# Kernel tuning notes

Hardware: AMD Instinct MI355X
Metric: run time of the kernel (lower is better)

Reference implementation:

```python
import jax, jax.numpy as jnp
from jax import lax
import numpy as np

B, T, H = 128, 512, 512  # batch, seq_length, hidden_dim (== input_dim)


def _xavier(key, shape):
    fan_in, fan_out = shape[1], shape[0]
    limit = float(np.sqrt(6.0 / (fan_in + fan_out)))
    return jax.random.uniform(key, shape, jnp.float32, -limit, limit)


def setup_inputs() -> dict:
    key = jax.random.key(0)
    ks = jax.random.split(key, 10)
    s = 1.0 / np.sqrt(H)  # torch LSTM default init range
    return {
        "x": jax.random.normal(ks[0], (B, T, H), jnp.float32),
        "W_ih": jax.random.uniform(ks[1], (4 * H, H), jnp.float32, -s, s),
        "W_hh": jax.random.uniform(ks[2], (4 * H, H), jnp.float32, -s, s),
        "b_ih": jax.random.uniform(ks[3], (4 * H,), jnp.float32, -s, s),
        "b_hh": jax.random.uniform(ks[4], (4 * H,), jnp.float32, -s, s),
        "Ve": _xavier(ks[5], (1, H)),
        "U1": _xavier(ks[6], (H, 2 * H)),
        "U2": _xavier(ks[7], (H, H)),
        "W_out": _xavier(ks[8], (2, H)),
        "b_out": jnp.zeros((2,), jnp.float32),
    }


def _lstm(x, W_ih, W_hh, b_ih, b_hh):
    # x: [B, T, D] -> hidden states [B, T, H]; PyTorch gate order i,f,g,o
    b = b_ih + b_hh
    # precompute input projections for all timesteps: [T, B, 4H]
    xg = jnp.einsum('btd,gd->tbg', x, W_ih) + b

    def step(carry, xt):
        h, c = carry
        g = xt + h @ W_hh.T  # [B, 4H]
        i, f, gg, o = jnp.split(g, 4, axis=1)
        c = jax.nn.sigmoid(f) * c + jax.nn.sigmoid(i) * jnp.tanh(gg)
        h = jax.nn.sigmoid(o) * jnp.tanh(c)
        return (h, c), h

    h0 = jnp.zeros((x.shape[0], W_hh.shape[1]), x.dtype)
    (_, _), hs = lax.scan(step, (h0, h0), xg)
    return jnp.swapaxes(hs, 0, 1)  # [B, T, H]


def reference(x, W_ih, W_hh, b_ih, b_hh, Ve, U1, U2, W_out, b_out):
    h = _lstm(x, W_ih, W_hh, b_ih, b_hh)  # [B, T, H]
    h_last = h[:, -1, :]  # [B, H]
    # additive attention, vectorized over all timesteps
    Hdim = h.shape[-1]
    u1 = jnp.einsum('bth,gh->btg', h, U1[:, :Hdim]) + jnp.einsum('bh,gh->bg', h_last, U1[:, Hdim:])[:, None, :]
    u2 = jnp.einsum('btd,gd->btg', x, U2)
    u = jnp.tanh(u1 + u2)  # [B, T, H]
    e = jnp.einsum('bth,h->bt', u, Ve[0])
    alpha = jax.nn.softmax(e, axis=1)  # [B, T]
    context = jnp.einsum('bt,bth->bh', alpha, h)  # [B, H]
    params = context @ W_out.T + b_out  # [B, 2]
    mu = params[:, 0]
    sigma = jax.nn.softplus(params[:, 1]) + 1e-5
    return (mu, sigma)
```

## Files before the change

kernel.cpp:

```cpp
#include <hip/hip_runtime.h>
#include <stdint.h>


using short8  = __attribute__((ext_vector_type(8))) short;
using short4v = __attribute__((ext_vector_type(4))) short;
using floatx4 = __attribute__((ext_vector_type(4))) float;

#define MFMA16(a, b, c) __builtin_amdgcn_mfma_f32_16x16x32_bf16((a), (b), (c), 0, 0, 0)

__device__ __forceinline__ unsigned short f2b(float f) {
    unsigned u = __float_as_uint(f);
    u += 0x7FFFu + ((u >> 16) & 1u);
    return (unsigned short)(u >> 16);
}
__device__ __forceinline__ float b2f(unsigned short h) {
    return __uint_as_float(((unsigned)h) << 16);
}
__device__ __forceinline__ float sigm(float x) { return 1.0f / (1.0f + __expf(-x)); }
__device__ __forceinline__ float tanh_(float x) { return 1.0f - 2.0f / (__expf(2.0f * x) + 1.0f); }

__global__ __launch_bounds__(256) void prep(
    const float* __restrict__ x, const float* __restrict__ Wih, const float* __restrict__ Whh,
    const float* __restrict__ bih, const float* __restrict__ bhh,
    const float* __restrict__ U1, const float* __restrict__ U2,
    unsigned short* __restrict__ x_bf, unsigned short* __restrict__ Wih_bf,
    unsigned short* __restrict__ Whh_bf, unsigned short* __restrict__ U1a,
    unsigned short* __restrict__ U1b, unsigned short* __restrict__ U2b,
    float* __restrict__ bias)
{
    const long long NX4 = 33554432LL / 4;
    const long long NREST = 1048576LL + 1048576LL + 524288LL + 262144LL + 2048LL;
    const long long total = NX4 + NREST;
    for (long long u = (long long)blockIdx.x * 256 + threadIdx.x; u < total;
         u += (long long)gridDim.x * 256) {
        if (u < NX4) {
            float4 v = ((const float4*)x)[u];
            short4v o;
            o[0] = (short)f2b(v.x); o[1] = (short)f2b(v.y);
            o[2] = (short)f2b(v.z); o[3] = (short)f2b(v.w);
            *(short4v*)&x_bf[u * 4] = o;
        } else {
            long long i = u - NX4;
            if (i < 1048576) { Wih_bf[i] = f2b(Wih[i]); continue; }
            i -= 1048576;
            if (i < 1048576) { Whh_bf[i] = f2b(Whh[i]); continue; }
            i -= 1048576;
            if (i < 524288) {
                int row = (int)(i >> 10), col = (int)(i & 1023);
                if (col < 512) U1a[row * 512 + col] = f2b(U1[i]);
                else           U1b[row * 512 + (col - 512)] = f2b(U1[i]);
                continue;
            }
            i -= 524288;
            if (i < 262144) { U2b[i] = f2b(U2[i]); continue; }
            i -= 262144;
            bias[i] = bih[i] + bhh[i];
        }
    }
}

__global__ __launch_bounds__(256) void gemm_bt(
    const unsigned short* __restrict__ A, long long lda,
    const unsigned short* __restrict__ Bm, long long ldb,
    unsigned short* __restrict__ C, long long ldc,
    const float* __restrict__ bias, int mode)
{
    __shared__ __align__(16) unsigned short sbuf[2 * 128 * 72];
    unsigned short* At = sbuf;
    unsigned short* Bt = sbuf + 128 * 72;
    unsigned short* Ct = sbuf;

    const int m0 = blockIdx.x * 128, n0 = blockIdx.y * 128;
    const int tid = threadIdx.x;
    const int wv = tid >> 6, lane = tid & 63, l15 = lane & 15, q = lane >> 4;
    const int wm = wv & 1, wn = wv >> 1;

    floatx4 acc[4][4];
    for (int i = 0; i < 4; i++)
        for (int j = 0; j < 4; j++) acc[i][j] = (floatx4){0.f, 0.f, 0.f, 0.f};

    for (int k0 = 0; k0 < 512; k0 += 64) {
        for (int p = 0; p < 4; p++) {
            int idx = tid + p * 256;
            int row = idx >> 3, ch = idx & 7;
            *(short8*)&At[row * 72 + ch * 8] =
                *(const short8*)&A[(long long)(m0 + row) * lda + k0 + ch * 8];
            *(short8*)&Bt[row * 72 + ch * 8] =
                *(const short8*)&Bm[(long long)(n0 + row) * ldb + k0 + ch * 8];
        }
        __syncthreads();
        for (int ks = 0; ks < 64; ks += 32) {
            short8 af[4], bfv[4];
            for (int mi = 0; mi < 4; mi++)
                af[mi] = *(const short8*)&At[(wm * 64 + mi * 16 + l15) * 72 + ks + q * 8];
            for (int ni = 0; ni < 4; ni++)
                bfv[ni] = *(const short8*)&Bt[(wn * 64 + ni * 16 + l15) * 72 + ks + q * 8];
            for (int mi = 0; mi < 4; mi++)
                for (int ni = 0; ni < 4; ni++)
                    acc[mi][ni] = MFMA16(af[mi], bfv[ni], acc[mi][ni]);
        }
        __syncthreads();
    }

    float bv[4];
    for (int ni = 0; ni < 4; ni++)
        bv[ni] = bias ? bias[n0 + wn * 64 + ni * 16 + l15] : 0.0f;

    for (int mi = 0; mi < 4; mi++)
        for (int ni = 0; ni < 4; ni++)
            for (int r = 0; r < 4; r++)
                Ct[(wm * 64 + mi * 16 + q * 4 + r) * 128 + wn * 64 + ni * 16 + l15] =
                    f2b(acc[mi][ni][r] + bv[ni]);
    __syncthreads();

    const int tt0 = m0 & 511, bglob = m0 >> 9;
    for (int p = 0; p < 8; p++) {
        int idx = tid + p * 256;
        int row = idx >> 4, ch = idx & 15;
        if (mode) {
            int n = n0 + ch * 8;
            int gate = n >> 9, jg = (n >> 4) & 31, c0 = gate * 16 + (n & 15);
            long long dst = (((long long)(tt0 + row) * 32 + jg) * 128 + bglob) * 64 + c0;
            *(short8*)&C[dst] = *(const short8*)&Ct[row * 128 + ch * 8];
        } else {
            *(short8*)&C[(long long)(m0 + row) * ldc + n0 + ch * 8] =
                *(const short8*)&Ct[row * 128 + ch * 8];
        }
    }
}

__global__ __launch_bounds__(256, 1) void lstm_rec(
    const unsigned short* __restrict__ xg,
    const unsigned short* __restrict__ Whh,
    unsigned short* __restrict__ h_all,
    unsigned int* __restrict__ ring)
{
    __shared__ unsigned int At[2][16 * 264];

    const int tid = threadIdx.x;
    const int wv = tid >> 6, lane = tid & 63, l15 = lane & 15, q = lane >> 4;
    const int bg = blockIdx.x >> 3, jgb = blockIdx.x & 7;
    const int b0 = bg * 16;
    const int jg32 = jgb * 4 + wv;
    const int hid = jg32 * 16 + l15;

    short8 Wreg[4][16];
    #pragma unroll
    for (int ct = 0; ct < 4; ct++)
        #pragma unroll
        for (int kk = 0; kk < 16; kk++)
            Wreg[ct][kk] = *(const short8*)
                &Whh[(long long)(ct * 512 + hid) * 512 + kk * 32 + q * 8];

    float cst[4] = {0.f, 0.f, 0.f, 0.f};

    for (int t = 0; t < 512; t++) {
        const long long xbase = ((long long)(t * 32 + jg32) * 128 + b0) * 64;
        floatx4 acc[4];
        #pragma unroll
        for (int ct = 0; ct < 4; ct++)
            #pragma unroll
            for (int r = 0; r < 4; r++)
                acc[ct][r] = b2f(xg[xbase + (q * 4 + r) * 64 + ct * 16 + l15]);

        if (t > 0) {
            const unsigned want = (unsigned)(t - 1);
            const int sl = (t - 1) & 1;
            unsigned long long* rb = (unsigned long long*)
                (ring + sl * 65536 + b0 * 512);
            unsigned long long w[16];
            #pragma unroll
            for (int i = 0; i < 16; i++)
                w[i] = __hip_atomic_load(&rb[tid + i * 256], __ATOMIC_RELAXED,
                                         __HIP_MEMORY_SCOPE_AGENT);
            while (true) {
                unsigned bad = 0;
                #pragma unroll
                for (int i = 0; i < 16; i++) {
                    unsigned lo = (unsigned)(w[i] >> 16) & 0xFFFFu;
                    unsigned hi = (unsigned)(w[i] >> 48);
                    bad |= (lo ^ want) | (hi ^ want);
                }
                if (!bad) break;
                #pragma unroll
                for (int i = 0; i < 16; i++) {
                    unsigned lo = (unsigned)(w[i] >> 16) & 0xFFFFu;
                    unsigned hi = (unsigned)(w[i] >> 48);
                    if ((lo ^ want) | (hi ^ want))
                        w[i] = __hip_atomic_load(&rb[tid + i * 256], __ATOMIC_RELAXED,
                                                 __HIP_MEMORY_SCOPE_AGENT);
                }
            }
            unsigned int* dst = &At[sl][0];
            #pragma unroll
            for (int i = 0; i < 16; i++) {
                int idx = tid + i * 256;
                int row = idx >> 8, k = idx & 255;
                dst[row * 264 + k] =
                    (unsigned)(w[i] & 0xFFFFu) | ((unsigned)(w[i] >> 32) << 16);
            }
            __syncthreads();
            const unsigned int* ap = &At[sl][l15 * 264 + q * 4];
            #pragma unroll
            for (int kk = 0; kk < 16; kk++) {
                short8 af = *(const short8*)(ap + kk * 16);
                acc[0] = MFMA16(af, Wreg[0][kk], acc[0]);
                acc[1] = MFMA16(af, Wreg[1][kk], acc[1]);
                acc[2] = MFMA16(af, Wreg[2][kk], acc[2]);
                acc[3] = MFMA16(af, Wreg[3][kk], acc[3]);
            }
        }
        unsigned short hbv[4];
        #pragma unroll
        for (int r = 0; r < 4; r++) {
            float ig = sigm(acc[0][r]);
            float fg = sigm(acc[1][r]);
            float gv = tanh_(acc[2][r]);
            float og = sigm(acc[3][r]);
            cst[r] = fg * cst[r] + ig * gv;
            hbv[r] = f2b(og * tanh_(cst[r]));
        }
        #pragma unroll
        for (int r = 0; r < 4; r++) {
            const int b = b0 + q * 4 + r;
            __hip_atomic_store(&ring[(t & 1) * 65536 + b * 512 + hid],
                               ((unsigned)t << 16) | hbv[r], __ATOMIC_RELAXED,
                               __HIP_MEMORY_SCOPE_AGENT);
        }
        #pragma unroll
        for (int r = 0; r < 4; r++) {
            const int b = b0 + q * 4 + r;
            h_all[(long long)b * 262144 + (long long)t * 512 + hid] = hbv[r];
        }
    }
}

__global__ __launch_bounds__(256) void attn_e(
    const unsigned short* __restrict__ h_all,
    const unsigned short* __restrict__ x_bf,
    const unsigned short* __restrict__ U1a, const unsigned short* __restrict__ U2b,
    const unsigned short* __restrict__ u1b,
    const float* __restrict__ Ve,
    float* __restrict__ e)
{
    __shared__ __align__(16) unsigned short Bt[512 * 40];
    __shared__ __align__(16) unsigned short At[32 * 40];
    __shared__ float ered[4][32];

    const int tid = threadIdx.x;
    const int wv = tid >> 6, lane = tid & 63, l15 = lane & 15, q = lane >> 4;
    const int b = blockIdx.x >> 4, t0 = (blockIdx.x & 15) * 32;

    floatx4 acc[2][8];
    for (int mi = 0; mi < 2; mi++)
        for (int ni = 0; ni < 8; ni++) acc[mi][ni] = (floatx4){0.f, 0.f, 0.f, 0.f};

    for (int it = 0; it < 32; it++) {
        const int phase = it >> 4, kk = (it & 15) * 32;
        const unsigned short* Asrc = phase ? x_bf : h_all;
        const unsigned short* Bsrc = phase ? U2b : U1a;
        __syncthreads();
        for (int idx = tid; idx < 2048; idx += 256) {
            int row = idx >> 2, ch = idx & 3;
            *(short8*)&Bt[row * 40 + ch * 8] =
                *(const short8*)&Bsrc[(long long)row * 512 + kk + ch * 8];
        }
        if (tid < 128) {
            int row = tid >> 2, ch = tid & 3;
            *(short8*)&At[row * 40 + ch * 8] =
                *(const short8*)&Asrc[(long long)(b * 512 + t0 + row) * 512 + kk + ch * 8];
        }
        __syncthreads();
        short8 af[2];
        for (int mi = 0; mi < 2; mi++)
            af[mi] = *(const short8*)&At[(mi * 16 + l15) * 40 + q * 8];
        for (int ni = 0; ni < 8; ni++) {
            short8 bfv = *(const short8*)&Bt[(wv * 128 + ni * 16 + l15) * 40 + q * 8];
            acc[0][ni] = MFMA16(af[0], bfv, acc[0][ni]);
            acc[1][ni] = MFMA16(af[1], bfv, acc[1][ni]);
        }
    }

    float s[2][4] = {{0.f, 0.f, 0.f, 0.f}, {0.f, 0.f, 0.f, 0.f}};
    for (int ni = 0; ni < 8; ni++) {
        int n = wv * 128 + ni * 16 + l15;
        float ub = b2f(u1b[b * 512 + n]);
        float vev = Ve[n];
        for (int mi = 0; mi < 2; mi++)
            for (int r = 0; r < 4; r++)
                s[mi][r] += vev * tanh_(acc[mi][ni][r] + ub);
    }
    for (int off = 1; off <= 8; off <<= 1)
        for (int mi = 0; mi < 2; mi++)
            for (int r = 0; r < 4; r++) s[mi][r] += __shfl_xor(s[mi][r], off);
    if (l15 == 0)
        for (int mi = 0; mi < 2; mi++)
            for (int r = 0; r < 4; r++) ered[wv][mi * 16 + q * 4 + r] = s[mi][r];
    __syncthreads();
    if (tid < 32)
        e[(long long)b * 512 + t0 + tid] =
            ered[0][tid] + ered[1][tid] + ered[2][tid] + ered[3][tid];
}

__global__ __launch_bounds__(256) void attn_out(
    const float* __restrict__ e, const unsigned short* __restrict__ h_all,
    const float* __restrict__ Wout, const float* __restrict__ bout,
    float* __restrict__ outp)
{
    __shared__ float sm[512];
    __shared__ float red[8];
    const int b = blockIdx.x, tid = threadIdx.x;
    const int wv = tid >> 6, lane = tid & 63;

    float e0 = e[b * 512 + tid], e1 = e[b * 512 + 256 + tid];
    float mx = fmaxf(e0, e1);
    for (int off = 32; off; off >>= 1) mx = fmaxf(mx, __shfl_xor(mx, off));
    if (lane == 0) red[wv] = mx;
    __syncthreads();
    mx = fmaxf(fmaxf(red[0], red[1]), fmaxf(red[2], red[3]));

    float s0 = __expf(e0 - mx), s1 = __expf(e1 - mx);
    sm[tid] = s0; sm[256 + tid] = s1;
    float ss = s0 + s1;
    for (int off = 32; off; off >>= 1) ss += __shfl_xor(ss, off);
    if (lane == 0) red[4 + wv] = ss;
    __syncthreads();
    float inv = 1.0f / (red[4] + red[5] + red[6] + red[7]);

    const long long base = (long long)b * 262144;
    float a0 = 0.f, a1 = 0.f;
    for (int t = 0; t < 512; t++) {
        float al = sm[t];
        a0 += al * b2f(h_all[base + t * 512 + tid]);
        a1 += al * b2f(h_all[base + t * 512 + 256 + tid]);
    }
    a0 *= inv; a1 *= inv;

    float q0 = a0 * Wout[tid] + a1 * Wout[256 + tid];
    float q1 = a0 * Wout[512 + tid] + a1 * Wout[768 + tid];
    for (int off = 32; off; off >>= 1) { q0 += __shfl_xor(q0, off); q1 += __shfl_xor(q1, off); }
    __syncthreads();
    if (lane == 0) { red[wv] = q0; red[4 + wv] = q1; }
    __syncthreads();
    if (tid == 0) {
        float P0 = red[0] + red[1] + red[2] + red[3] + bout[0];
        float P1 = red[4] + red[5] + red[6] + red[7] + bout[1];
        outp[b] = P0;
        float sp = (P1 > 15.0f) ? P1 : log1pf(__expf(P1));
        outp[128 + b] = sp + 1e-5f;
    }
}

extern "C" void kernel_launch(void* const* d_in, const int* in_sizes, int n_in,
                              void* d_out, int out_size, void* d_ws, size_t ws_size,
                              hipStream_t stream)
{
    const float* x    = (const float*)d_in[0];
    const float* Wih  = (const float*)d_in[1];
    const float* Whh  = (const float*)d_in[2];
    const float* bih  = (const float*)d_in[3];
    const float* bhh  = (const float*)d_in[4];
    const float* Ve   = (const float*)d_in[5];
    const float* U1   = (const float*)d_in[6];
    const float* U2   = (const float*)d_in[7];
    const float* Wout = (const float*)d_in[8];
    const float* bout = (const float*)d_in[9];
    float* out = (float*)d_out;

    char* ws = (char*)d_ws;
    size_t off = 0;
    auto alloc = [&](size_t bytes) -> void* {
        void* p = ws + off;
        off += (bytes + 255) & ~(size_t)255;
        return p;
    };
    unsigned short* x_bf   = (unsigned short*)alloc(33554432ull * 2);
    unsigned short* Wih_bf = (unsigned short*)alloc(1048576ull * 2);
    unsigned short* Whh_bf = (unsigned short*)alloc(1048576ull * 2);
    unsigned short* U1a    = (unsigned short*)alloc(262144ull * 2);
    unsigned short* U1b    = (unsigned short*)alloc(262144ull * 2);
    unsigned short* U2b    = (unsigned short*)alloc(262144ull * 2);
    float*          bias   = (float*)alloc(2048ull * 4);
    unsigned short* xg     = (unsigned short*)alloc(134217728ull * 2);
    unsigned short* h_all  = (unsigned short*)alloc(33554432ull * 2);
    unsigned short* u1bv   = (unsigned short*)alloc(65536ull * 2);
    float*          e      = (float*)alloc(65536ull * 4);
    unsigned int*   ring   = (unsigned int*)alloc(131072ull * 4);
    if (off > ws_size) return;

    prep<<<4096, 256, 0, stream>>>(x, Wih, Whh, bih, bhh, U1, U2,
                                   x_bf, Wih_bf, Whh_bf, U1a, U1b, U2b, bias);
    gemm_bt<<<dim3(512, 16), 256, 0, stream>>>(x_bf, 512, Wih_bf, 512,
                                               xg, 2048, bias, 1);
    lstm_rec<<<64, 256, 0, stream>>>(xg, Whh_bf, h_all, ring);
    gemm_bt<<<dim3(1, 4), 256, 0, stream>>>(h_all + 511 * 512, 262144, U1b, 512,
                                            u1bv, 512, nullptr, 0);
    attn_e<<<2048, 256, 0, stream>>>(h_all, x_bf, U1a, U2b, u1bv, Ve, e);
    attn_out<<<128, 256, 0, stream>>>(e, h_all, Wout, bout, out);
}
```

Before: 2.809 ms.

## Process two batch groups per LSTM recurrence block, halving the grid

```diff
diff --git a/kernel.cpp b/kernel.cpp
--- a/kernel.cpp
+++ b/kernel.cpp
@@ -139,8 +139,7 @@
 
     const int tid = threadIdx.x;
     const int wv = tid >> 6, lane = tid & 63, l15 = lane & 15, q = lane >> 4;
-    const int bg = blockIdx.x >> 3, jgb = blockIdx.x & 7;
-    const int b0 = bg * 16;
+    const int pair = blockIdx.x >> 3, jgb = blockIdx.x & 7;
     const int jg32 = jgb * 4 + wv;
     const int hid = jg32 * 16 + l15;
 
@@ -152,85 +151,101 @@
             Wreg[ct][kk] = *(const short8*)
                 &Whh[(long long)(ct * 512 + hid) * 512 + kk * 32 + q * 8];
 
-    float cst[4] = {0.f, 0.f, 0.f, 0.f};
+    float cst[2][4] = {{0.f, 0.f, 0.f, 0.f}, {0.f, 0.f, 0.f, 0.f}};
 
     for (int t = 0; t < 512; t++) {
-        const long long xbase = ((long long)(t * 32 + jg32) * 128 + b0) * 64;
-        floatx4 acc[4];
+        float xv[2][16];
         #pragma unroll
-        for (int ct = 0; ct < 4; ct++)
+        for (int hf = 0; hf < 2; hf++) {
+            const int b0 = (pair + hf * 4) * 16;
+            const long long xbase = ((long long)(t * 32 + jg32) * 128 + b0) * 64;
             #pragma unroll
-            for (int r = 0; r < 4; r++)
-                acc[ct][r] = b2f(xg[xbase + (q * 4 + r) * 64 + ct * 16 + l15]);
-
-        if (t > 0) {
-            const unsigned want = (unsigned)(t - 1);
-            const int sl = (t - 1) & 1;
-            unsigned long long* rb = (unsigned long long*)
-                (ring + sl * 65536 + b0 * 512);
-            unsigned long long w[16];
+            for (int ct = 0; ct < 4; ct++)
+                #pragma unroll
+                for (int r = 0; r < 4; r++)
+                    xv[hf][ct * 4 + r] =
+                        b2f(xg[xbase + (q * 4 + r) * 64 + ct * 16 + l15]);
+        }
+
+        #pragma unroll
+        for (int hf = 0; hf < 2; hf++) {
+            const int b0 = (pair + hf * 4) * 16;
+            floatx4 acc[4];
             #pragma unroll
-            for (int i = 0; i < 16; i++)
-                w[i] = __hip_atomic_load(&rb[tid + i * 256], __ATOMIC_RELAXED,
-                                         __HIP_MEMORY_SCOPE_AGENT);
-            while (true) {
-                unsigned bad = 0;
+            for (int ct = 0; ct < 4; ct++)
+                #pragma unroll
+                for (int r = 0; r < 4; r++)
+                    acc[ct][r] = xv[hf][ct * 4 + r];
+
+            if (t > 0) {
+                const unsigned want = (unsigned)(t - 1);
+                const int sl = (t - 1) & 1;
+                unsigned long long* rb = (unsigned long long*)
+                    (ring + sl * 65536 + b0 * 512);
+                unsigned long long w[16];
+                #pragma unroll
+                for (int i = 0; i < 16; i++)
+                    w[i] = __hip_atomic_load(&rb[tid + i * 256], __ATOMIC_RELAXED,
+                                             __HIP_MEMORY_SCOPE_AGENT);
+                while (true) {
+                    unsigned bad = 0;
+                    #pragma unroll
+                    for (int i = 0; i < 16; i++) {
+                        unsigned lo = (unsigned)(w[i] >> 16) & 0xFFFFu;
+                        unsigned hi = (unsigned)(w[i] >> 48);
+                        bad |= (lo ^ want) | (hi ^ want);
+                    }
+                    if (!bad) break;
+                    #pragma unroll
+                    for (int i = 0; i < 16; i++) {
+                        unsigned lo = (unsigned)(w[i] >> 16) & 0xFFFFu;
+                        unsigned hi = (unsigned)(w[i] >> 48);
+                        if ((lo ^ want) | (hi ^ want))
+                            w[i] = __hip_atomic_load(&rb[tid + i * 256], __ATOMIC_RELAXED,
+                                                     __HIP_MEMORY_SCOPE_AGENT);
+                    }
+                }
+                unsigned int* dst = &At[hf][0];
                 #pragma unroll
                 for (int i = 0; i < 16; i++) {
-                    unsigned lo = (unsigned)(w[i] >> 16) & 0xFFFFu;
-                    unsigned hi = (unsigned)(w[i] >> 48);
-                    bad |= (lo ^ want) | (hi ^ want);
+                    int idx = tid + i * 256;
+                    int row = idx >> 8, k = idx & 255;
+                    dst[row * 264 + k] =
+                        (unsigned)(w[i] & 0xFFFFu) | ((unsigned)(w[i] >> 32) << 16);
                 }
-                if (!bad) break;
+                __syncthreads();
+                const unsigned int* ap = &At[hf][l15 * 264 + q * 4];
                 #pragma unroll
-                for (int i = 0; i < 16; i++) {
-                    unsigned lo = (unsigned)(w[i] >> 16) & 0xFFFFu;
-                    unsigned hi = (unsigned)(w[i] >> 48);
-                    if ((lo ^ want) | (hi ^ want))
-                        w[i] = __hip_atomic_load(&rb[tid + i * 256], __ATOMIC_RELAXED,
-                                                 __HIP_MEMORY_SCOPE_AGENT);
+                for (int kk = 0; kk < 16; kk++) {
+                    short8 af = *(const short8*)(ap + kk * 16);
+                    acc[0] = MFMA16(af, Wreg[0][kk], acc[0]);
+                    acc[1] = MFMA16(af, Wreg[1][kk], acc[1]);
+                    acc[2] = MFMA16(af, Wreg[2][kk], acc[2]);
+                    acc[3] = MFMA16(af, Wreg[3][kk], acc[3]);
                 }
             }
-            unsigned int* dst = &At[sl][0];
+            unsigned short hbv[4];
             #pragma unroll
-            for (int i = 0; i < 16; i++) {
-                int idx = tid + i * 256;
-                int row = idx >> 8, k = idx & 255;
-                dst[row * 264 + k] =
-                    (unsigned)(w[i] & 0xFFFFu) | ((unsigned)(w[i] >> 32) << 16);
+            for (int r = 0; r < 4; r++) {
+                float ig = sigm(acc[0][r]);
+                float fg = sigm(acc[1][r]);
+                float gv = tanh_(acc[2][r]);
+                float og = sigm(acc[3][r]);
+                cst[hf][r] = fg * cst[hf][r] + ig * gv;
+                hbv[r] = f2b(og * tanh_(cst[hf][r]));
             }
-            __syncthreads();
-            const unsigned int* ap = &At[sl][l15 * 264 + q * 4];
             #pragma unroll
-            for (int kk = 0; kk < 16; kk++) {
-                short8 af = *(const short8*)(ap + kk * 16);
-                acc[0] = MFMA16(af, Wreg[0][kk], acc[0]);
-                acc[1] = MFMA16(af, Wreg[1][kk], acc[1]);
-                acc[2] = MFMA16(af, Wreg[2][kk], acc[2]);
-                acc[3] = MFMA16(af, Wreg[3][kk], acc[3]);
+            for (int r = 0; r < 4; r++) {
+                const int b = b0 + q * 4 + r;
+                __hip_atomic_store(&ring[(t & 1) * 65536 + b * 512 + hid],
+                                   ((unsigned)t << 16) | hbv[r], __ATOMIC_RELAXED,
+                                   __HIP_MEMORY_SCOPE_AGENT);
             }
-        }
-        unsigned short hbv[4];
-        #pragma unroll
-        for (int r = 0; r < 4; r++) {
-            float ig = sigm(acc[0][r]);
-            float fg = sigm(acc[1][r]);
-            float gv = tanh_(acc[2][r]);
-            float og = sigm(acc[3][r]);
-            cst[r] = fg * cst[r] + ig * gv;
-            hbv[r] = f2b(og * tanh_(cst[r]));
-        }
-        #pragma unroll
-        for (int r = 0; r < 4; r++) {
-            const int b = b0 + q * 4 + r;
-            __hip_atomic_store(&ring[(t & 1) * 65536 + b * 512 + hid],
-                               ((unsigned)t << 16) | hbv[r], __ATOMIC_RELAXED,
-                               __HIP_MEMORY_SCOPE_AGENT);
-        }
-        #pragma unroll
-        for (int r = 0; r < 4; r++) {
-            const int b = b0 + q * 4 + r;
-            h_all[(long long)b * 262144 + (long long)t * 512 + hid] = hbv[r];
+            #pragma unroll
+            for (int r = 0; r < 4; r++) {
+                const int b = b0 + q * 4 + r;
+                h_all[(long long)b * 262144 + (long long)t * 512 + hid] = hbv[r];
+            }
         }
     }
 }
@@ -392,7 +407,7 @@
                                    x_bf, Wih_bf, Whh_bf, U1a, U1b, U2b, bias);
     gemm_bt<<<dim3(512, 16), 256, 0, stream>>>(x_bf, 512, Wih_bf, 512,
                                                xg, 2048, bias, 1);
-    lstm_rec<<<64, 256, 0, stream>>>(xg, Whh_bf, h_all, ring);
+    lstm_rec<<<32, 256, 0, stream>>>(xg, Whh_bf, h_all, ring);
     gemm_bt<<<dim3(1, 4), 256, 0, stream>>>(h_all + 511 * 512, 262144, U1b, 512,
                                             u1bv, 512, nullptr, 0);
     attn_e<<<2048, 256, 0, stream>>>(h_all, x_bf, U1a, U2b, u1bv, Ve, e);
```

After: 4.331 ms. +54.2%, slower.

## Overlap input-projection GEMM with LSTM recurrence in a combined kernel

Applied to the files above, without the earlier changes.

```diff
diff --git a/kernel.cpp b/kernel.cpp
--- a/kernel.cpp
+++ b/kernel.cpp
@@ -59,19 +59,17 @@
     }
 }
 
-__global__ __launch_bounds__(256) void gemm_bt(
+__device__ __forceinline__ void gemm_core(
     const unsigned short* __restrict__ A, long long lda,
     const unsigned short* __restrict__ Bm, long long ldb,
     unsigned short* __restrict__ C, long long ldc,
-    const float* __restrict__ bias, int mode)
-{
-    __shared__ __align__(16) unsigned short sbuf[2 * 128 * 72];
+    const float* __restrict__ bias, int mode,
+    int m0, int n0, int tid, unsigned short* sbuf)
+{
     unsigned short* At = sbuf;
     unsigned short* Bt = sbuf + 128 * 72;
     unsigned short* Ct = sbuf;
 
-    const int m0 = blockIdx.x * 128, n0 = blockIdx.y * 128;
-    const int tid = threadIdx.x;
     const int wv = tid >> 6, lane = tid & 63, l15 = lane & 15, q = lane >> 4;
     const int wm = wv & 1, wn = wv >> 1;
 
@@ -129,15 +127,50 @@
     }
 }
 
-__global__ __launch_bounds__(256, 1) void lstm_rec(
+__global__ __launch_bounds__(256) void gemm_bt(
+    const unsigned short* __restrict__ A, long long lda,
+    const unsigned short* __restrict__ Bm, long long ldb,
+    unsigned short* __restrict__ C, long long ldc,
+    const float* __restrict__ bias, int mode, int mmul)
+{
+    __shared__ __align__(16) unsigned short sbuf[2 * 128 * 72];
+    gemm_core(A, lda, Bm, ldb, C, ldc, bias, mode,
+              blockIdx.x * mmul, blockIdx.y * 128, threadIdx.x, sbuf);
+}
+
+#define GEMM_WGS 6144
+__global__ __launch_bounds__(256, 1) void mega(
     const unsigned short* __restrict__ xg,
     const unsigned short* __restrict__ Whh,
     unsigned short* __restrict__ h_all,
-    unsigned int* __restrict__ ring)
-{
-    __shared__ unsigned int At[2][16 * 264];
+    unsigned int* __restrict__ ring,
+    const unsigned short* __restrict__ x_bf,
+    const unsigned short* __restrict__ Wih_bf,
+    const float* __restrict__ bias,
+    unsigned short* __restrict__ xg_out,
+    int* __restrict__ done)
+{
+    __shared__ __align__(16) char smem[36864];
 
     const int tid = threadIdx.x;
+
+    if (blockIdx.x >= 64) {
+        int g = blockIdx.x - 64;
+        int b = g & 127;
+        int r = g >> 7;
+        int ti = 1 + (r % 3);
+        int n = r / 3;
+        gemm_core(x_bf, 512, Wih_bf, 512, xg_out, 2048, bias, 1,
+                  b * 512 + ti * 128, n * 128, tid, (unsigned short*)smem);
+        __syncthreads();
+        if (tid == 0)
+            __hip_atomic_fetch_add(done, 1, __ATOMIC_RELEASE,
+                                   __HIP_MEMORY_SCOPE_AGENT);
+        return;
+    }
+
+    unsigned int (*At)[16 * 264] = (unsigned int (*)[16 * 264])smem;
+
     const int wv = tid >> 6, lane = tid & 63, l15 = lane & 15, q = lane >> 4;
     const int bg = blockIdx.x >> 3, jgb = blockIdx.x & 7;
     const int b0 = bg * 16;
@@ -155,6 +188,14 @@
     float cst[4] = {0.f, 0.f, 0.f, 0.f};
 
     for (int t = 0; t < 512; t++) {
+        if (t == 128) {
+            if (tid == 0) {
+                while (__hip_atomic_load(done, __ATOMIC_ACQUIRE,
+                                         __HIP_MEMORY_SCOPE_AGENT) < GEMM_WGS)
+                    __builtin_amdgcn_s_sleep(8);
+            }
+            __syncthreads();
+        }
         const long long xbase = ((long long)(t * 32 + jg32) * 128 + b0) * 64;
         floatx4 acc[4];
         #pragma unroll
@@ -327,17 +368,21 @@
     __syncthreads();
     float inv = 1.0f / (red[4] + red[5] + red[6] + red[7]);
 
-    const long long base = (long long)b * 262144;
+    const unsigned int* hp = (const unsigned int*)(h_all + (long long)b * 262144);
     float a0 = 0.f, a1 = 0.f;
-    for (int t = 0; t < 512; t++) {
-        float al = sm[t];
-        a0 += al * b2f(h_all[base + t * 512 + tid]);
-        a1 += al * b2f(h_all[base + t * 512 + 256 + tid]);
+    for (int t = 0; t < 512; t += 4) {
+        #pragma unroll
+        for (int j = 0; j < 4; j++) {
+            float al = sm[t + j];
+            unsigned v = hp[(t + j) * 256 + tid];
+            a0 += al * b2f((unsigned short)(v & 0xFFFFu));
+            a1 += al * b2f((unsigned short)(v >> 16));
+        }
     }
     a0 *= inv; a1 *= inv;
 
-    float q0 = a0 * Wout[tid] + a1 * Wout[256 + tid];
-    float q1 = a0 * Wout[512 + tid] + a1 * Wout[768 + tid];
+    float q0 = a0 * Wout[2 * tid] + a1 * Wout[2 * tid + 1];
+    float q1 = a0 * Wout[512 + 2 * tid] + a1 * Wout[512 + 2 * tid + 1];
     for (int off = 32; off; off >>= 1) { q0 += __shfl_xor(q0, off); q1 += __shfl_xor(q1, off); }
     __syncthreads();
     if (lane == 0) { red[wv] = q0; red[4 + wv] = q1; }
@@ -386,15 +431,18 @@
     unsigned short* u1bv   = (unsigned short*)alloc(65536ull * 2);
     float*          e      = (float*)alloc(65536ull * 4);
     unsigned int*   ring   = (unsigned int*)alloc(131072ull * 4);
+    int*            done   = (int*)alloc(256ull);
     if (off > ws_size) return;
 
+    hipMemsetAsync(done, 0, 4, stream);
     prep<<<4096, 256, 0, stream>>>(x, Wih, Whh, bih, bhh, U1, U2,
                                    x_bf, Wih_bf, Whh_bf, U1a, U1b, U2b, bias);
-    gemm_bt<<<dim3(512, 16), 256, 0, stream>>>(x_bf, 512, Wih_bf, 512,
-                                               xg, 2048, bias, 1);
-    lstm_rec<<<64, 256, 0, stream>>>(xg, Whh_bf, h_all, ring);
+    gemm_bt<<<dim3(128, 16), 256, 0, stream>>>(x_bf, 512, Wih_bf, 512,
+                                               xg, 2048, bias, 1, 512);
+    mega<<<64 + GEMM_WGS, 256, 0, stream>>>(xg, Whh_bf, h_all, ring,
+                                            x_bf, Wih_bf, bias, xg, done);
     gemm_bt<<<dim3(1, 4), 256, 0, stream>>>(h_all + 511 * 512, 262144, U1b, 512,
-                                            u1bv, 512, nullptr, 0);
+                                            u1bv, 512, nullptr, 0, 128);
     attn_e<<<2048, 256, 0, stream>>>(h_all, x_bf, U1a, U2b, u1bv, Ve, e);
     attn_out<<<128, 256, 0, stream>>>(e, h_all, Wout, bout, out);
 }
```

Result: faster. 2.752 ms (-2.0%).
